# Kernel tuning notes

Measured on AMD Instinct MI355X. Metric: run time of the kernel, lower is better.

The kernel has to match this reference:

```python
import jax, jax.numpy as jnp
import numpy as np

B, T, C = 512, 55, 512     # batch, seq_len (max_len=55 eval), input_size
D, K, L, OUT = 512, 64, 3, 512  # embedding_size, k_size, num_layers, output_size
ALPHA = 1.0 / L


def setup_inputs() -> dict:
    key = jax.random.key(0)
    ks = jax.random.split(key, 32)
    def p(k, shape, fan_in):
        return jax.random.normal(k, shape, dtype=jnp.float32) * (1.0 / np.sqrt(fan_in))
    inp = {}
    inp["inputs"] = jax.random.normal(ks[0], (B, T, C), dtype=jnp.float32)
    inp["init_keys"] = jax.random.uniform(ks[1], (B, K), dtype=jnp.float32)
    ki = 2
    for l in range(L):
        fin = C + l * D  # growing concat input width
        inp[f"wx{l}_w"] = p(ks[ki], (fin, 4 * D), fin); ki += 1
        inp[f"wx{l}_b"] = jnp.zeros((4 * D,), jnp.float32)
        inp[f"wh{l}_w"] = p(ks[ki], (D, 4 * D), D); ki += 1
        inp[f"wh{l}_b"] = jnp.zeros((4 * D,), jnp.float32)
        inp[f"wr{l}_w"] = p(ks[ki], (fin, K), fin); ki += 1
        inp[f"wl{l}_w"] = p(ks[ki], (D, K), D); ki += 1
    inp["wd_w"] = p(ks[ki], (K, D), K); ki += 1
    inp["proj_w"] = p(ks[ki], (L * D, OUT), L * D); ki += 1
    inp["proj_b"] = jnp.zeros((OUT,), jnp.float32)
    return inp


def _forward(inputs, init_keys, wx_w, wx_b, wh_w, wh_b, wr_w, wl_w, wd_w, proj_w, proj_b):
    Bv = inputs.shape[0]
    h0 = tuple(jnp.zeros((Bv, D), inputs.dtype) for _ in range(L))
    c0 = tuple(jnp.zeros((Bv, D), inputs.dtype) for _ in range(L))
    d0 = tuple(init_keys for _ in range(L))

    def step(carry, x_t):
        hs, cs, ds = carry
        xt = x_t  # [B, C]; grows by D per layer
        nh, nc, nd = [], [], []
        for l in range(L):
            gate = xt @ wx_w[l] + wx_b[l] + hs[l] @ wh_w[l] + wh_b[l]  # [B, 4D]
            f = jax.nn.sigmoid(gate[:, :D])
            i = jax.nn.sigmoid(gate[:, D:2 * D])
            o = jax.nn.sigmoid(gate[:, 2 * D:3 * D])
            cbar = jnp.tanh(gate[:, 3 * D:])
            gr = xt @ wr_w[l]  # [B, K]
            for j in range(l):
                gr = gr + ALPHA * (hs[j] @ wl_w[j])
            r = jax.nn.sigmoid(gr)
            d_new = r * ds[l]                               # [B, K]
            c = f * cs[l] + i * cbar + jnp.tanh(d_new @ wd_w)  # [B, D]
            h = o * jnp.tanh(c)
            xt = jnp.concatenate([xt, h], axis=-1)
            nh.append(h); nc.append(c); nd.append(d_new)
        out = jnp.concatenate(nh, axis=-1) @ proj_w + proj_b  # [B, OUT]
        return (tuple(nh), tuple(nc), tuple(nd)), out

    _, outs = jax.lax.scan(step, (h0, c0, d0), jnp.swapaxes(inputs, 0, 1))  # [T, B, OUT]
    return jnp.swapaxes(outs, 0, 1)  # [B, T, OUT]


def reference(inputs, init_keys, wx0_w, wx0_b, wx1_w, wx1_b, wx2_w, wx2_b,
              wh0_w, wh0_b, wh1_w, wh1_b, wh2_w, wh2_b,
              wr0_w, wr1_w, wr2_w, wl0_w, wl1_w, wl2_w,
              wd_w, proj_w, proj_b):
    return _forward(inputs, init_keys,
                    (wx0_w, wx1_w, wx2_w), (wx0_b, wx1_b, wx2_b),
                    (wh0_w, wh1_w, wh2_w), (wh0_b, wh1_b, wh2_b),
                    (wr0_w, wr1_w, wr2_w), (wl0_w, wl1_w, wl2_w),
                    wd_w, proj_w, proj_b)
```

## Files before the change

### kernel.cpp

```cpp
#include <hip/hip_runtime.h>
#include <hip/hip_bf16.h>

typedef __hip_bfloat16 bf16;
typedef __attribute__((ext_vector_type(8))) short s16x8;
typedef __attribute__((ext_vector_type(4))) float f32x4;

#define TT 55
#define BB 512
#define DD 512
#define KK 64
#define NHS 8
#define LDH ((long)NHS*1536)

typedef const __attribute__((address_space(1))) unsigned int gu32;
typedef __attribute__((address_space(3))) unsigned int lu32;
__device__ __forceinline__ void gload16(const void* g, void* l) {
  __builtin_amdgcn_global_load_lds((gu32*)g, (lu32*)l, 16, 0, 0);
}

struct Seg {
  void*  dst;
  long   ldd;
  int    col_begin;
  int    mode;
  const float* bias;
};
struct SegList { Seg s[4]; int n; };

struct GDesc {
  const bf16* Ap[4]; const bf16* B;
  long ldap[4], ldb;
  int mtiles, ntiles, tile_beg, K;
  SegList segs;
};
struct GArgs { GDesc g[4]; int ng; int total; int chunk; };

__global__ __launch_bounds__(256) void gemm_batched(GArgs args)
{
  __shared__ __align__(16) bf16 As[2][64][64];
  __shared__ __align__(16) bf16 Bs[2][64][64];

  int tile = (int)(blockIdx.x & 7) * args.chunk + (int)(blockIdx.x >> 3);
  if (tile >= args.total) return;

  int gi = 0;
  for (int i = 1; i < args.ng; ++i) if (tile >= args.g[i].tile_beg) gi = i;
  const GDesc& g = args.g[gi];
  const int local = tile - g.tile_beg;
  const int mt = local % g.mtiles;
  const int nt = local / g.mtiles;

  const int tid  = threadIdx.x;
  const int wave = tid >> 6, lane = tid & 63;
  const int q = lane >> 4, mm = lane & 15;
  const int s7 = mm & 7;
  const int wm = wave >> 1, wn = wave & 1;
  const long m0 = (long)mt * 64;
  const long n0 = (long)nt * 64;

  const bf16* Bb = g.B + n0 * g.ldb;
  const long ldb = g.ldb;
  const int l8 = lane >> 3;
  const int gc = ((lane & 7) ^ l8) << 3;

  const int nk = g.K >> 6;

  auto stage = [&](int b, int k0) {
    const int p = k0 >> 9;
    const long ldap = g.ldap[p];
    const bf16* Abp = g.Ap[p] + m0 * ldap;
    const int ko = k0 & 511;
#pragma unroll
    for (int pp = 0; pp < 2; ++pp) {
      int r = pp*32 + wave*8;
      gload16(Abp + (long)(r + l8)*ldap + ko + gc, &As[b][r][0]);
    }
#pragma unroll
    for (int pp = 0; pp < 2; ++pp) {
      int r = pp*32 + wave*8;
      gload16(Bb + (long)(r + l8)*ldb + k0 + gc, &Bs[b][r][0]);
    }
  };

  f32x4 acc[2][2] = {};

  stage(0, 0);
  asm volatile("s_waitcnt vmcnt(0)" ::: "memory");
  __builtin_amdgcn_s_barrier();

  for (int k = 0; k < nk; ++k) {
    const int cur = k & 1;
    if (k + 1 < nk) stage(cur ^ 1, (k + 1) << 6);
#pragma unroll
    for (int kk = 0; kk < 64; kk += 32) {
      const int pc = ((((kk >> 3) + q) ^ s7) << 3);
      s16x8 av[2], bv[2];
#pragma unroll
      for (int i = 0; i < 2; ++i) av[i] = *(const s16x8*)&As[cur][wm*32 + i*16 + mm][pc];
#pragma unroll
      for (int j = 0; j < 2; ++j) bv[j] = *(const s16x8*)&Bs[cur][wn*32 + j*16 + mm][pc];
#pragma unroll
      for (int i = 0; i < 2; ++i)
#pragma unroll
        for (int j = 0; j < 2; ++j)
          acc[i][j] = __builtin_amdgcn_mfma_f32_16x16x32_bf16(av[i], bv[j], acc[i][j], 0,0,0);
    }
    if (k + 1 < nk) {
      asm volatile("s_waitcnt vmcnt(0)" ::: "memory");
      __builtin_amdgcn_s_barrier();
    }
  }

  Seg sg = g.segs.s[0];
  for (int i = 1; i < g.segs.n; ++i)
    if ((int)n0 >= g.segs.s[i].col_begin) sg = g.segs.s[i];
#pragma unroll
  for (int j = 0; j < 2; ++j) {
    int dcol = (int)n0 + wn*32 + j*16 + mm - sg.col_begin;
    float bv = sg.bias ? sg.bias[dcol] : 0.0f;
#pragma unroll
    for (int i = 0; i < 2; ++i) {
      f32x4 a = acc[i][j];
#pragma unroll
      for (int r = 0; r < 4; ++r) {
        long row = m0 + wm*32 + i*16 + q*4 + r;
        ((float*)sg.dst)[row * sg.ldd + dcol] = a[r] + bv;
      }
    }
  }
}

struct CellDesc {
  const float* gate;
  const float* gr;
  const float* u0;
  const float* u1;
  float* c;
  float* d;
  bf16*  hout;
};
struct CArgs { CellDesc e[3]; int n; };

__device__ inline float sigm(float x){ return 1.0f/(1.0f + __expf(-x)); }
__device__ inline float ftanh(float x){ float e = __expf(2.0f*x); return 1.0f - 2.0f/(e + 1.0f); }

__global__ __launch_bounds__(256) void cell_batched(CArgs a, const float* __restrict__ wd)
{
  const CellDesc e = a.e[blockIdx.y];
  const int tid = threadIdx.x;
  const int r0 = blockIdx.x * 2;
  __shared__ float dn[2][64];

  if (tid < 128) {
    int r = tid >> 6, k = tid & 63;
    long row = r0 + r;
    float gv = e.gr[row*64 + k];
    if (e.u0) gv += (1.0f/3.0f)*e.u0[row*64 + k];
    if (e.u1) gv += (1.0f/3.0f)*e.u1[row*64 + k];
    float rr = sigm(gv);
    float dv = rr * e.d[row*64 + k];
    e.d[row*64 + k] = dv;
    dn[r][k] = dv;
  }
  __syncthreads();

  float accv[2][2] = {};
#pragma unroll 4
  for (int k = 0; k < 64; ++k) {
    float w0 = wd[k*512 + tid];
    float w1 = wd[k*512 + tid + 256];
#pragma unroll
    for (int r = 0; r < 2; ++r) {
      float dv = dn[r][k];
      accv[0][r] += dv * w0;
      accv[1][r] += dv * w1;
    }
  }

#pragma unroll
  for (int half = 0; half < 2; ++half) {
    int n = tid + half*256;
#pragma unroll
    for (int r = 0; r < 2; ++r) {
      long row = r0 + r;
      const float* gg = e.gate + row*2048;
      float fv = sigm(gg[n]);
      float iv = sigm(gg[512+n]);
      float ov = sigm(gg[1024+n]);
      float cb = ftanh(gg[1536+n]);
      float cv = fv * e.c[row*512 + n] + iv * cb + ftanh(accv[half][r]);
      e.c[row*512 + n] = cv;
      e.hout[row*LDH + n] = __float2bfloat16(ov * ftanh(cv));
    }
  }
}

__global__ void k_tpose2(const float* __restrict__ src, long srow,
                         bf16* __restrict__ dst, long drow, int kcnt, long koff,
                         long total)
{
  long idx = (long)blockIdx.x * 256 + threadIdx.x;
  if (idx >= total) return;
  long n = idx / kcnt;
  long k = idx - n * kcnt;
  dst[n*drow + koff + k] = __float2bfloat16(src[k * srow + n]);
}

__global__ void k_xconv(const float* __restrict__ x, bf16* __restrict__ xb)
{
  long i = (long)blockIdx.x * 256 + threadIdx.x;
  if (i >= (long)TT*BB*512) return;
  int cc = (int)(i & 511);
  long r = i >> 9;
  int t = (int)(r / BB), b = (int)(r - (long)t*BB);
  xb[i] = __float2bfloat16(x[((long)b*TT + t)*512 + cc]);
}

__global__ void k_bias(const float* b0,const float* b1,const float* b2,
                       const float* b3,const float* b4,const float* b5,
                       float* out)
{
  int i = blockIdx.x*256 + threadIdx.x;
  if (i < 2048)      out[i] = b0[i] + b1[i];
  else if (i < 4096) out[i] = b2[i-2048] + b3[i-2048];
  else if (i < 6144) out[i] = b4[i-4096] + b5[i-4096];
}

__global__ void k_dinit(const float* __restrict__ keys, float* __restrict__ d)
{
  int i = blockIdx.x*256 + threadIdx.x;
  if (i < 3*BB*KK) d[i] = keys[i % (BB*KK)];
}

extern "C" void kernel_launch(void* const* d_in, const int* in_sizes, int n_in,
                              void* d_out, int out_size, void* d_ws, size_t ws_size,
                              hipStream_t stream)
{
  const float* inputs    = (const float*)d_in[0];
  const float* init_keys = (const float*)d_in[1];
  const float* wx_w[3] = {(const float*)d_in[2],  (const float*)d_in[8],  (const float*)d_in[14]};
  const float* wx_b[3] = {(const float*)d_in[3],  (const float*)d_in[9],  (const float*)d_in[15]};
  const float* wh_w[3] = {(const float*)d_in[4],  (const float*)d_in[10], (const float*)d_in[16]};
  const float* wh_b[3] = {(const float*)d_in[5],  (const float*)d_in[11], (const float*)d_in[17]};
  const float* wr_w[3] = {(const float*)d_in[6],  (const float*)d_in[12], (const float*)d_in[18]};
  const float* wl_w[3] = {(const float*)d_in[7],  (const float*)d_in[13], (const float*)d_in[19]};
  const float* wd_w   = (const float*)d_in[20];
  const float* proj_w = (const float*)d_in[21];
  const float* proj_b = (const float*)d_in[22];
  float* out = (float*)d_out;

  char* wsp = (char*)d_ws;
  size_t used = 0;
  auto alloc = [&](size_t bytes) {
    char* p = wsp + used;
    used += (bytes + 255) & ~(size_t)255;
    return p;
  };
  bf16* xb    = (bf16*)alloc((size_t)TT*BB*512*2);
  bf16* WL0T  = (bf16*)alloc((size_t)2176*1024*2);
  bf16* WL1T  = (bf16*)alloc((size_t)2176*1536*2);
  bf16* WL2T  = (bf16*)alloc((size_t)2176*2048*2);
  bf16* projT = (bf16*)alloc((size_t)512*1536*2);
  bf16* HallR = (bf16*)alloc((size_t)BB*NHS*1536*2);
  bf16* hz    = (bf16*)alloc((size_t)BB*512*2);
  float* accg = (float*)alloc((size_t)4*3*BB*2048*4);
  float* accr = (float*)alloc((size_t)4*3*BB*64*4);
  float* ubuf = (float*)alloc((size_t)4*2*BB*64*4);
  float* cbuf = (float*)alloc((size_t)3*BB*DD*4);
  float* dbuf = (float*)alloc((size_t)3*BB*KK*4);
  float* biasg= (float*)alloc((size_t)3*2048*4);
  float* dump = (float*)alloc((size_t)BB*64*4);
  if (used > ws_size) return;

  const long SZG = (long)BB*2048;
  const long SZR = (long)BB*64;

  auto slotg = [&](int s, int l){ return accg + (long)((s&3)*3+l)*SZG; };
  auto slotr = [&](int s, int l){ return accr + (long)((s&3)*3+l)*SZR; };
  auto slotu = [&](int s, int j){ return ubuf + (long)((s&3)*2+j)*SZR; };
  auto hb    = [&](int s){ return HallR + (long)(s % NHS)*1536; };

  {
    long tot = (long)TT*BB*512;
    k_xconv<<<dim3((tot + 255)/256), 256, 0, stream>>>(inputs, xb);
  }
  hipMemsetAsync(WL0T, 0, (size_t)2176*1024*2, stream);
  hipMemsetAsync(WL1T, 0, (size_t)2176*1536*2, stream);
  hipMemsetAsync(WL2T, 0, (size_t)2176*2048*2, stream);
  hipMemsetAsync(hz,   0, (size_t)BB*512*2, stream);
  hipMemsetAsync(cbuf, 0, (size_t)3*BB*DD*4, stream);

  auto tp2 = [&](const float* src, long kOffSrc, long srow,
                 bf16* dst, long colbase, long drow, long koff, int N){
    long total = (long)N*512;
    k_tpose2<<<dim3((total + 255)/256), 256, 0, stream>>>(
        src + kOffSrc*srow, srow, dst + colbase*drow, drow, 512, koff, total);
  };
  tp2(wx_w[0],0,2048, WL0T,0,1024,0,2048);
  tp2(wh_w[0],0,2048, WL0T,0,1024,512,2048);
  tp2(wr_w[0],0,64,   WL0T,2048,1024,0,64);
  tp2(wl_w[0],0,64,   WL0T,2112,1024,512,64);
  tp2(wx_w[1],0,2048,   WL1T,0,1536,0,2048);
  tp2(wx_w[1],512,2048, WL1T,0,1536,512,2048);
  tp2(wh_w[1],0,2048,   WL1T,0,1536,1024,2048);
  tp2(wr_w[1],0,64,     WL1T,2048,1536,0,64);
  tp2(wr_w[1],512,64,   WL1T,2048,1536,512,64);
  tp2(wl_w[1],0,64,     WL1T,2112,1536,1024,64);
  tp2(wx_w[2],0,2048,    WL2T,0,2048,0,2048);
  tp2(wx_w[2],512,2048,  WL2T,0,2048,512,2048);
  tp2(wx_w[2],1024,2048, WL2T,0,2048,1024,2048);
  tp2(wh_w[2],0,2048,    WL2T,0,2048,1536,2048);
  tp2(wr_w[2],0,64,      WL2T,2048,2048,0,64);
  tp2(wr_w[2],512,64,    WL2T,2048,2048,512,64);
  tp2(wr_w[2],1024,64,   WL2T,2048,2048,1024,64);
  {
    long total = (long)512*1536;
    k_tpose2<<<dim3((total + 255)/256), 256, 0, stream>>>(
        proj_w, 512, projT, 1536, 1536, 0, total);
  }

  k_bias<<<dim3(24),256,0,stream>>>(wx_b[0],wh_b[0],wx_b[1],wh_b[1],wx_b[2],wh_b[2], biasg);
  k_dinit<<<dim3((3*BB*KK + 255)/256),256,0,stream>>>(init_keys, dbuf);

  for (int t = -1; t <= TT + 1; ++t) {
    CArgs ca{}; ca.n = 0;
    auto addE = [&](int s, int l){
      CellDesc& e = ca.e[ca.n++];
      e.gate = slotg(s,l);
      e.gr   = slotr(s,l);
      e.u0 = (l>=1) ? slotu(s-1,0) : nullptr;
      e.u1 = (l>=2) ? slotu(s-1,1) : nullptr;
      e.c = cbuf + (long)l*BB*DD; e.d = dbuf + (long)l*BB*KK;
      e.hout = hb(s) + (long)l*512;
    };
    if (t   >= 0 && t   < TT) addE(t,   0);
    if (t-1 >= 0 && t-1 < TT) addE(t-1, 1);
    if (t-2 >= 0 && t-2 < TT) addE(t-2, 2);
    if (ca.n)
      cell_batched<<<dim3(256, ca.n), 256, 0, stream>>>(ca, wd_w);

    GArgs ga{}; ga.ng = 0;
    int cursor = 0;
    auto addG = [&](const bf16* B, long ldb, int ntiles, int Kd, SegList sl,
                    const bf16* a0, long l0, const bf16* a1, long l1,
                    const bf16* a2, long l2, const bf16* a3, long l3){
      GDesc& g = ga.g[ga.ng++];
      g.Ap[0]=a0; g.Ap[1]=a1; g.Ap[2]=a2; g.Ap[3]=a3;
      g.ldap[0]=l0; g.ldap[1]=l1; g.ldap[2]=l2; g.ldap[3]=l3;
      g.B = B; g.ldb = ldb;
      g.mtiles = 8; g.ntiles = ntiles; g.tile_beg = cursor; g.K = Kd;
      cursor += 8 * ntiles;
      g.segs = sl;
    };
    if (t >= -1 && t <= TT-2) {
      SegList sl{}; sl.n = 3;
      sl.s[0] = { slotg(t+1,0), 2048,    0, 0, biasg + 0 };
      sl.s[1] = { slotr(t+1,0),   64, 2048, 0, nullptr   };
      sl.s[2] = { slotu(t,0),     64, 2112, 0, nullptr   };
      addG(WL0T, 1024, 34, 1024, sl,
           xb + (long)(t+1)*BB*512, 512,
           (t>=0)? hb(t) : hz, (t>=0)? LDH : 512,
           nullptr,0, nullptr,0);
    }
    if (t >= 0 && t <= TT-1) {
      SegList sl{}; sl.n = 3;
      sl.s[0] = { slotg(t,1),   2048,    0, 0, biasg + 2048 };
      sl.s[1] = { slotr(t,1),     64, 2048, 0, nullptr      };
      sl.s[2] = { slotu(t-1,1),   64, 2112, 0, nullptr      };
      addG(WL1T, 1536, 34, 1536, sl,
           xb + (long)t*BB*512, 512,
           hb(t), LDH,
           (t>=1)? hb(t-1)+512 : hz, (t>=1)? LDH : 512,
           nullptr,0);
    }
    if (t >= 1 && t <= TT) {
      int s = t-1;
      SegList sl{}; sl.n = 3;
      sl.s[0] = { slotg(s,2), 2048,    0, 0, biasg + 4096 };
      sl.s[1] = { slotr(s,2),   64, 2048, 0, nullptr      };
      sl.s[2] = { dump,         64, 2112, 0, nullptr      };
      addG(WL2T, 2048, 34, 2048, sl,
           xb + (long)s*BB*512, 512,
           hb(s), LDH,
           hb(s)+512, LDH,
           (s>=1)? hb(s-1)+1024 : hz, (s>=1)? LDH : 512);
    }
    if (t-2 >= 0 && t-2 < TT) {
      int s = t-2;
      SegList sl{}; sl.n = 1;
      sl.s[0] = { out + (long)s*512, (long)TT*512, 0, 0, proj_b };
      addG(projT, 1536, 8, 1536, sl,
           hb(s), LDH, hb(s)+512, LDH, hb(s)+1024, LDH, nullptr,0);
    }
    if (cursor) {
      ga.total = cursor; ga.chunk = (cursor + 7) / 8;
      gemm_batched<<<dim3(ga.chunk * 8), 256, 0, stream>>>(ga);
    }
  }
}
```

Before: 2.555 ms.

## Hoist output projection out of recurrence into one batched GEMM over all timesteps

Hidden states are now kept for every timestep in a full [B,T,1536] buffer instead of an 8-slot ring. The per-step projection GEMM is dropped from the time loop and replaced by a single large GEMM over all B*T rows after the recurrence, writing directly into the output layout. This shortens each per-step batched launch and gives the projection much better occupancy, at the cost of a larger workspace. The GEMM inner loop is also reworked so the barrier and partial vmcnt wait come after issuing the next stage's prefetch, letting loads overlap compute.

```diff
diff --git a/kernel.cpp b/kernel.cpp
--- a/kernel.cpp
+++ b/kernel.cpp
@@ -9,8 +9,7 @@
 #define BB 512
 #define DD 512
 #define KK 64
-#define NHS 8
-#define LDH ((long)NHS*1536)
+#define LDH ((long)TT*1536)
 
 typedef const __attribute__((address_space(1))) unsigned int gu32;
 typedef __attribute__((address_space(3))) unsigned int lu32;
@@ -85,12 +84,15 @@
   f32x4 acc[2][2] = {};
 
   stage(0, 0);
-  asm volatile("s_waitcnt vmcnt(0)" ::: "memory");
-  __builtin_amdgcn_s_barrier();
-
   for (int k = 0; k < nk; ++k) {
     const int cur = k & 1;
-    if (k + 1 < nk) stage(cur ^ 1, (k + 1) << 6);
+    if (k + 1 < nk) {
+      stage(cur ^ 1, (k + 1) << 6);
+      asm volatile("s_waitcnt vmcnt(4)" ::: "memory");
+    } else {
+      asm volatile("s_waitcnt vmcnt(0)" ::: "memory");
+    }
+    __builtin_amdgcn_s_barrier();
 #pragma unroll
     for (int kk = 0; kk < 64; kk += 32) {
       const int pc = ((((kk >> 3) + q) ^ s7) << 3);
@@ -105,10 +107,7 @@
         for (int j = 0; j < 2; ++j)
           acc[i][j] = __builtin_amdgcn_mfma_f32_16x16x32_bf16(av[i], bv[j], acc[i][j], 0,0,0);
     }
-    if (k + 1 < nk) {
-      asm volatile("s_waitcnt vmcnt(0)" ::: "memory");
-      __builtin_amdgcn_s_barrier();
-    }
+    __builtin_amdgcn_s_barrier();
   }
 
   Seg sg = g.segs.s[0];
@@ -261,7 +260,7 @@
   bf16* WL1T  = (bf16*)alloc((size_t)2176*1536*2);
   bf16* WL2T  = (bf16*)alloc((size_t)2176*2048*2);
   bf16* projT = (bf16*)alloc((size_t)512*1536*2);
-  bf16* HallR = (bf16*)alloc((size_t)BB*NHS*1536*2);
+  bf16* Hall  = (bf16*)alloc((size_t)BB*TT*1536*2);
   bf16* hz    = (bf16*)alloc((size_t)BB*512*2);
   float* accg = (float*)alloc((size_t)4*3*BB*2048*4);
   float* accr = (float*)alloc((size_t)4*3*BB*64*4);
@@ -278,7 +277,7 @@
   auto slotg = [&](int s, int l){ return accg + (long)((s&3)*3+l)*SZG; };
   auto slotr = [&](int s, int l){ return accr + (long)((s&3)*3+l)*SZR; };
   auto slotu = [&](int s, int j){ return ubuf + (long)((s&3)*2+j)*SZR; };
-  auto hb    = [&](int s){ return HallR + (long)(s % NHS)*1536; };
+  auto hb    = [&](int s){ return Hall + (long)s*1536; };
 
   {
     long tot = (long)TT*BB*512;
@@ -341,15 +340,15 @@
 
     GArgs ga{}; ga.ng = 0;
     int cursor = 0;
-    auto addG = [&](const bf16* B, long ldb, int ntiles, int Kd, SegList sl,
+    auto addG = [&](const bf16* B, long ldb, int mtiles, int ntiles, int Kd, SegList sl,
                     const bf16* a0, long l0, const bf16* a1, long l1,
                     const bf16* a2, long l2, const bf16* a3, long l3){
       GDesc& g = ga.g[ga.ng++];
       g.Ap[0]=a0; g.Ap[1]=a1; g.Ap[2]=a2; g.Ap[3]=a3;
       g.ldap[0]=l0; g.ldap[1]=l1; g.ldap[2]=l2; g.ldap[3]=l3;
       g.B = B; g.ldb = ldb;
-      g.mtiles = 8; g.ntiles = ntiles; g.tile_beg = cursor; g.K = Kd;
-      cursor += 8 * ntiles;
+      g.mtiles = mtiles; g.ntiles = ntiles; g.tile_beg = cursor; g.K = Kd;
+      cursor += mtiles * ntiles;
       g.segs = sl;
     };
     if (t >= -1 && t <= TT-2) {
@@ -357,7 +356,7 @@
       sl.s[0] = { slotg(t+1,0), 2048,    0, 0, biasg + 0 };
       sl.s[1] = { slotr(t+1,0),   64, 2048, 0, nullptr   };
       sl.s[2] = { slotu(t,0),     64, 2112, 0, nullptr   };
-      addG(WL0T, 1024, 34, 1024, sl,
+      addG(WL0T, 1024, 8, 34, 1024, sl,
            xb + (long)(t+1)*BB*512, 512,
            (t>=0)? hb(t) : hz, (t>=0)? LDH : 512,
            nullptr,0, nullptr,0);
@@ -367,7 +366,7 @@
       sl.s[0] = { slotg(t,1),   2048,    0, 0, biasg + 2048 };
       sl.s[1] = { slotr(t,1),     64, 2048, 0, nullptr      };
       sl.s[2] = { slotu(t-1,1),   64, 2112, 0, nullptr      };
-      addG(WL1T, 1536, 34, 1536, sl,
+      addG(WL1T, 1536, 8, 34, 1536, sl,
            xb + (long)t*BB*512, 512,
            hb(t), LDH,
            (t>=1)? hb(t-1)+512 : hz, (t>=1)? LDH : 512,
@@ -379,22 +378,30 @@
       sl.s[0] = { slotg(s,2), 2048,    0, 0, biasg + 4096 };
       sl.s[1] = { slotr(s,2),   64, 2048, 0, nullptr      };
       sl.s[2] = { dump,         64, 2112, 0, nullptr      };
-      addG(WL2T, 2048, 34, 2048, sl,
+      addG(WL2T, 2048, 8, 34, 2048, sl,
            xb + (long)s*BB*512, 512,
            hb(s), LDH,
            hb(s)+512, LDH,
            (s>=1)? hb(s-1)+1024 : hz, (s>=1)? LDH : 512);
     }
-    if (t-2 >= 0 && t-2 < TT) {
-      int s = t-2;
-      SegList sl{}; sl.n = 1;
-      sl.s[0] = { out + (long)s*512, (long)TT*512, 0, 0, proj_b };
-      addG(projT, 1536, 8, 1536, sl,
-           hb(s), LDH, hb(s)+512, LDH, hb(s)+1024, LDH, nullptr,0);
-    }
     if (cursor) {
       ga.total = cursor; ga.chunk = (cursor + 7) / 8;
       gemm_batched<<<dim3(ga.chunk * 8), 256, 0, stream>>>(ga);
     }
   }
-}
+
+  {
+    GArgs ga{}; ga.ng = 1;
+    GDesc& g = ga.g[0];
+    g.Ap[0] = Hall;        g.ldap[0] = 1536;
+    g.Ap[1] = Hall + 512;  g.ldap[1] = 1536;
+    g.Ap[2] = Hall + 1024; g.ldap[2] = 1536;
+    g.Ap[3] = nullptr;     g.ldap[3] = 0;
+    g.B = projT; g.ldb = 1536;
+    g.mtiles = (BB*TT)/64; g.ntiles = 8; g.tile_beg = 0; g.K = 1536;
+    g.segs.n = 1;
+    g.segs.s[0] = { out, 512, 0, 0, proj_b };
+    ga.total = g.mtiles * g.ntiles; ga.chunk = (ga.total + 7) / 8;
+    gemm_batched<<<dim3(ga.chunk * 8), 256, 0, stream>>>(ga);
+  }
+}
```

Result: no change. 2.549 ms (-0.2%).
